# Kernel tuning notes

Measured on AMD Instinct MI355X. Metric: run time of the kernel, lower is better.

## Reference

```python
import jax, jax.numpy as jnp
import numpy as np

N_NODES = 50000
N_EDGES = 800000
FEAT = 128
HID = 128
NUM_GRAPHS = 64
ODE_STEPS = 8   # fixed-step RK4 stand-in for adaptive odeint over CFG.ode_time_points
DEPTH = 1.0
EPS = 1e-5


def layer_norm(x, g, b):
    m = jnp.mean(x, axis=-1, keepdims=True)
    v = jnp.var(x, axis=-1, keepdims=True)
    return (x - m) * jax.lax.rsqrt(v + EPS) * g + b


def setup_inputs() -> dict:
    key = jax.random.key(0)
    ks = jax.random.split(key, 16)
    s = 1.0 / np.sqrt(FEAT)
    sh = 1.0 / np.sqrt(HID)
    inp = {
        "x": jax.random.normal(ks[0], (N_NODES, FEAT), jnp.float32),
        "edge_index": jax.random.randint(ks[1], (2, N_EDGES), 0, N_NODES, jnp.int64),
        "batch": jnp.sort(jax.random.randint(ks[2], (N_NODES,), 0, NUM_GRAPHS, jnp.int64)),
        "alpha": jnp.float32(0.8),
        "beta": jnp.float32(0.6),
        "phase": jnp.float32(0.7),
        "W_in": jax.random.normal(ks[3], (FEAT, HID), jnp.float32) * s,
        "b_in": jnp.zeros((HID,), jnp.float32),
        "g_in": jnp.ones((HID,), jnp.float32),
        "be_in": jnp.zeros((HID,), jnp.float32),
        "W_alt": jax.random.normal(ks[4], (FEAT, HID), jnp.float32) * s,
        "b_alt": jnp.zeros((HID,), jnp.float32),
        "g_alt": jnp.ones((HID,), jnp.float32),
        "be_alt": jnp.zeros((HID,), jnp.float32),
        "W_self": jax.random.normal(ks[5], (HID, HID), jnp.float32) * sh,
        "W_msg": jax.random.normal(ks[6], (HID, HID), jnp.float32) * sh,
        "b_ode": jnp.zeros((HID,), jnp.float32),
        "W_int": jax.random.normal(ks[7], (2 * HID, HID), jnp.float32) * sh / np.sqrt(2.0),
        "b_int": jnp.zeros((HID,), jnp.float32),
        "g_int": jnp.ones((HID,), jnp.float32),
        "be_int": jnp.zeros((HID,), jnp.float32),
        "W_out": jax.random.normal(ks[8], (HID, HID), jnp.float32) * sh,
        "b_out": jnp.zeros((HID,), jnp.float32),
    }
    return inp


def _forward(x, alpha, beta, phase,
             W_in, b_in, g_in, be_in,
             W_alt, b_alt, g_alt, be_alt,
             W_self, W_msg, b_ode,
             W_int, b_int, g_int, be_int,
             W_out, b_out,
             edge_index, batch):
    src, dst = edge_index[0], edge_index[1]
    # in-degree for mean aggregation (clamped to 1)
    deg = jax.ops.segment_sum(jnp.ones((src.shape[0],), jnp.float32), dst,
                              num_segments=N_NODES)
    deg = jnp.maximum(deg, 1.0)[:, None]

    # quantum amplitudes -> measurement probabilities (normalized)
    norm = jnp.sqrt(alpha ** 2 + beta ** 2)
    a, b = alpha / norm, beta / norm
    p0, p1 = a ** 2, b ** 2

    # two projection pathways in superposition
    h0 = jax.nn.gelu(layer_norm(x @ W_in + b_in, g_in, be_in))
    h1 = jax.nn.gelu(layer_norm(x @ W_alt + b_alt, g_alt, be_alt))
    h = jnp.sqrt(p0) * h0 + jnp.sqrt(p1) * h1  # [N, H]

    # Neural ODE: dh/dt = tanh(h W_self + mean_{j->i}(h_j W_msg) + b)
    def ode_f(h):
        msg = h[src] @ W_msg                       # [E, H] gather + GEMM
        agg = jax.ops.segment_sum(msg, dst, num_segments=N_NODES) / deg
        return jnp.tanh(h @ W_self + agg + b_ode)

    dt = jnp.float32(DEPTH / ODE_STEPS)

    def rk4_step(h, _):
        k1 = ode_f(h)
        k2 = ode_f(h + 0.5 * dt * k1)
        k3 = ode_f(h + 0.5 * dt * k2)
        k4 = ode_f(h + dt * k3)
        return h + (dt / 6.0) * (k1 + 2.0 * k2 + 2.0 * k3 + k4), None

    h, _ = jax.lax.scan(rk4_step, h, None, length=ODE_STEPS)

    # quantum interference mixing (conditional branch -> masked add)
    interf = 2.0 * jnp.sqrt(p0 * p1) * jnp.cos(phase)
    h_int = jnp.tanh(layer_norm(jnp.concatenate([h, h], axis=-1) @ W_int + b_int,
                                g_int, be_int))
    gate = jnp.where(jnp.abs(interf) > 0.01, interf, 0.0)
    h = h + gate * h_int

    # eval-mode collapse: if p1 >= p0, scale by Re(e^{i*phase}) = cos(phase)
    h = jnp.where(p0 > p1, h, h * jnp.cos(phase))

    h_out = h @ W_out + b_out

    # global mean pool over graphs
    cnt = jax.ops.segment_sum(jnp.ones((N_NODES,), jnp.float32), batch,
                              num_segments=NUM_GRAPHS)
    pooled = jax.ops.segment_sum(h_out, batch, num_segments=NUM_GRAPHS)
    return pooled / jnp.maximum(cnt, 1.0)[:, None]  # [NUM_GRAPHS, H]


def reference(x, edge_index, batch, alpha, beta, phase,
              W_in, b_in, g_in, be_in,
              W_alt, b_alt, g_alt, be_alt,
              W_self, W_msg, b_ode,
              W_int, b_int, g_int, be_int,
              W_out, b_out):
    return _forward(x, alpha, beta, phase,
                    W_in, b_in, g_in, be_in,
                    W_alt, b_alt, g_alt, be_alt,
                    W_self, W_msg, b_ode,
                    W_int, b_int, g_int, be_int,
                    W_out, b_out, edge_index, batch)
```

## Files before the change

### kernel.cpp

```cpp
#include <hip/hip_runtime.h>
#include <math.h>

#define NND 50000
#define NED 800000
#define HD  128
#define NG  64
#define MT  32

typedef __attribute__((ext_vector_type(8))) short short8v;
typedef __attribute__((ext_vector_type(4))) float float4v;
typedef __attribute__((ext_vector_type(2))) float float2v;

__device__ __forceinline__ float gelu_t(float x) {
  const float c = 0.7978845608028654f;
  float t = tanhf(c * (x + 0.044715f * x * x * x));
  return 0.5f * x * (1.0f + t);
}

__device__ __forceinline__ unsigned short f2bf(float f) {
  unsigned int u = __float_as_uint(f);
  u += 0x7FFFu + ((u >> 16) & 1u);
  return (unsigned short)(u >> 16);
}
__device__ __forceinline__ float bf2f(unsigned short s) {
  return __uint_as_float(((unsigned int)s) << 16);
}
__device__ __forceinline__ float bflo(unsigned int u) { return __uint_as_float(u << 16); }
__device__ __forceinline__ float bfhi(unsigned int u) { return __uint_as_float(u & 0xFFFF0000u); }
__device__ __forceinline__ unsigned char f2fp8(float f) {
  return (unsigned char)(__builtin_amdgcn_cvt_pk_fp8_f32(f, f, 0, false) & 0xFF);
}

__global__ void k_hist(const int* __restrict__ dst, int* __restrict__ degi) {
  int e = blockIdx.x * 256 + threadIdx.x;
  if (e < NED) atomicAdd(&degi[dst[e]], 1);
}

__global__ __launch_bounds__(1024) void k_scan(
    const int* __restrict__ degi, int* __restrict__ rowptr,
    int* __restrict__ cursor, float* __restrict__ deginv) {
  __shared__ int wsum[16];
  int tid = threadIdx.x;
  int lane = tid & 63;
  int wid = tid >> 6;
  int running = 0;
  for (int base = 0; base < NND; base += 1024) {
    int idx = base + tid;
    int v = (idx < NND) ? degi[idx] : 0;
    int s = v;
#pragma unroll
    for (int o = 1; o < 64; o <<= 1) {
      int t = __shfl_up(s, o, 64);
      if (lane >= o) s += t;
    }
    if (lane == 63) wsum[wid] = s;
    __syncthreads();
    if (wid == 0) {
      int ws = (lane < 16) ? wsum[lane] : 0;
#pragma unroll
      for (int o = 1; o < 16; o <<= 1) {
        int t = __shfl_up(ws, o, 64);
        if (lane >= o) ws += t;
      }
      if (lane < 16) wsum[lane] = ws;
    }
    __syncthreads();
    int woff = wid ? wsum[wid - 1] : 0;
    int excl = running + woff + s - v;
    if (idx < NND) {
      rowptr[idx] = excl;
      cursor[idx] = excl;
      deginv[idx] = 1.0f / (float)max(v, 1);
    }
    int tot = wsum[15];
    __syncthreads();
    running += tot;
  }
  if (tid == 0) rowptr[NND] = running;
}

__global__ void k_scatter(const int* __restrict__ src, const int* __restrict__ dst,
                          int* __restrict__ cursor, int* __restrict__ csrsrc) {
  int e = blockIdx.x * 256 + threadIdx.x;
  if (e < NED) {
    int d = dst[e];
    int pos = atomicAdd(&cursor[d], 1);
    csrsrc[pos] = src[e];
  }
}

__global__ void k_cnt(const int* __restrict__ batch, float* __restrict__ cnt) {
  int g = threadIdx.x;
  if (g >= NG) return;
  int lo, hi, ub_g, ub_gm1;
  lo = 0; hi = NND;
  while (lo < hi) { int mid = (lo + hi) >> 1; if (batch[mid] <= g) lo = mid + 1; else hi = mid; }
  ub_g = lo;
  if (g == 0) ub_gm1 = 0;
  else {
    lo = 0; hi = NND;
    int v = g - 1;
    while (lo < hi) { int mid = (lo + hi) >> 1; if (batch[mid] <= v) lo = mid + 1; else hi = mid; }
    ub_gm1 = lo;
  }
  cnt[g] = (float)(ub_g - ub_gm1);
}

__global__ void k_weff(const float* __restrict__ Wint, float* __restrict__ weff) {
  int i = blockIdx.x * 256 + threadIdx.x;
  if (i < HD * HD) weff[i] = Wint[i] + Wint[i + HD * HD];
}

__global__ void k_prepB(const float* __restrict__ Wself, const float* __restrict__ Wmsg,
                        unsigned short* __restrict__ Bt) {
  int i = blockIdx.x * 256 + threadIdx.x;
  if (i < 128 * 256) {
    int n = i >> 8, k = i & 255;
    float w = (k < HD) ? Wself[k * HD + n] : Wmsg[(k - HD) * HD + n];
    Bt[i] = f2bf(w);
  }
}

__global__ void k_prepIn(const float* __restrict__ Win, const float* __restrict__ Walt,
                         unsigned short* __restrict__ BtIn) {
  int i = blockIdx.x * 256 + threadIdx.x;
  if (i < 2 * 128 * 128) {
    int p = i >> 14; int rem = i & 16383; int n = rem >> 7; int k = rem & 127;
    const float* W = p ? Walt : Win;
    BtIn[i] = f2bf(W[k * 128 + n]);
  }
}

__global__ __launch_bounds__(256) void k_init2(
    const float* __restrict__ x, const unsigned short* __restrict__ BtIn,
    const float* __restrict__ bin, const float* __restrict__ gin, const float* __restrict__ bein,
    const float* __restrict__ balt, const float* __restrict__ galt, const float* __restrict__ bealt,
    const float* __restrict__ alphap, const float* __restrict__ betap,
    float* __restrict__ hdst, unsigned short* __restrict__ hbf)
{
  __shared__ float red[4][16][2];
  __shared__ unsigned short gtile[2][16][64];
  int tid = threadIdx.x;
  int wave = tid >> 6;
  int lane = tid & 63;
  int l15 = lane & 15;
  int lhi = lane >> 4;
  int path = wave >> 1;
  int colBase = (wave & 1) * 64;
  int rowBase = blockIdx.x * 64;

  const unsigned short* Bp = BtIn + path * 128 * 128;
  short8v bfr[4][4];
#pragma unroll
  for (int t = 0; t < 4; ++t) {
    int n = colBase + t * 16 + l15;
#pragma unroll
    for (int s = 0; s < 4; ++s)
      bfr[t][s] = *(const short8v*)&Bp[n * 128 + s * 32 + lhi * 8];
  }

  const float* bvp = path ? balt : bin;
  const float* gp  = path ? galt : gin;
  const float* bep = path ? bealt : bein;
  float bv[4], gw[4], bew[4];
#pragma unroll
  for (int t = 0; t < 4; ++t) {
    int col = colBase + t * 16 + l15;
    bv[t] = bvp[col]; gw[t] = gp[col]; bew[t] = bep[col];
  }

  float al = alphap[0], btv = betap[0];
  float nrm = sqrtf(al * al + btv * btv);
  float w0 = fabsf(al) / nrm, w1 = fabsf(btv) / nrm;

  for (int rt = 0; rt < 4; ++rt) {
    int arow = rowBase + rt * 16 + l15; if (arow >= NND) arow = NND - 1;
    short8v afr[4];
#pragma unroll
    for (int s = 0; s < 4; ++s) {
      float4 xa = *(const float4*)&x[(size_t)arow * HD + s * 32 + lhi * 8];
      float4 xb = *(const float4*)&x[(size_t)arow * HD + s * 32 + lhi * 8 + 4];
      short8v f;
      f[0] = (short)f2bf(xa.x); f[1] = (short)f2bf(xa.y);
      f[2] = (short)f2bf(xa.z); f[3] = (short)f2bf(xa.w);
      f[4] = (short)f2bf(xb.x); f[5] = (short)f2bf(xb.y);
      f[6] = (short)f2bf(xb.z); f[7] = (short)f2bf(xb.w);
      afr[s] = f;
    }

    float4v acc[4];
#pragma unroll
    for (int t = 0; t < 4; ++t) acc[t] = (float4v){0.f, 0.f, 0.f, 0.f};
#pragma unroll
    for (int s = 0; s < 4; ++s) {
#pragma unroll
      for (int t = 0; t < 4; ++t)
        acc[t] = __builtin_amdgcn_mfma_f32_16x16x32_bf16(afr[s], bfr[t][s], acc[t], 0, 0, 0);
    }

    float z[4][4];
    float psum[4], psq[4];
#pragma unroll
    for (int r = 0; r < 4; ++r) {
      float s1 = 0.f, s2 = 0.f;
#pragma unroll
      for (int t = 0; t < 4; ++t) {
        float zz = acc[t][r] + bv[t];
        z[r][t] = zz;
        s1 += zz; s2 += zz * zz;
      }
#pragma unroll
      for (int m = 1; m < 16; m <<= 1) {
        s1 += __shfl_xor(s1, m, 16);
        s2 += __shfl_xor(s2, m, 16);
      }
      psum[r] = s1; psq[r] = s2;
    }
    if (l15 == 0) {
#pragma unroll
      for (int r = 0; r < 4; ++r) {
        red[wave][lhi * 4 + r][0] = psum[r];
        red[wave][lhi * 4 + r][1] = psq[r];
      }
    }
    __syncthreads();

    int pw = wave ^ 1;
    float gval[4][4];
#pragma unroll
    for (int r = 0; r < 4; ++r) {
      int rowl = lhi * 4 + r;
      float S = psum[r] + red[pw][rowl][0];
      float Q = psq[r]  + red[pw][rowl][1];
      float mean = S * (1.0f / 128.0f);
      float var  = Q * (1.0f / 128.0f) - mean * mean;
      float rs = rsqrtf(var + 1e-5f);
#pragma unroll
      for (int t = 0; t < 4; ++t)
        gval[r][t] = gelu_t((z[r][t] - mean) * rs * gw[t] + bew[t]);
    }

    if (path == 1) {
#pragma unroll
      for (int r = 0; r < 4; ++r)
#pragma unroll
        for (int t = 0; t < 4; ++t)
          gtile[wave & 1][lhi * 4 + r][t * 16 + l15] = f2bf(gval[r][t]);
    }
    __syncthreads();

    if (path == 0) {
#pragma unroll
      for (int r = 0; r < 4; ++r) {
        int m = rowBase + rt * 16 + lhi * 4 + r;
        if (m < NND) {
#pragma unroll
          for (int t = 0; t < 4; ++t) {
            float g1 = bf2f(gtile[wave & 1][lhi * 4 + r][t * 16 + l15]);
            float hv = w0 * gval[r][t] + w1 * g1;
            size_t off = (size_t)m * HD + colBase + t * 16 + l15;
            hdst[off] = hv;
            hbf[off] = f2bf(hv);
          }
        }
      }
    }
    __syncthreads();
  }
}

__global__ __launch_bounds__(256) void k_fused(
    const unsigned short* __restrict__ ain,
    const unsigned short* __restrict__ hbf,
    const unsigned char* __restrict__ k8r,
    unsigned char* __restrict__ k8w,
    unsigned short* __restrict__ usav,
    unsigned short* __restrict__ kacc,
    const int* __restrict__ rowptr, const int* __restrict__ csrsrc,
    const float* __restrict__ deginv,
    const unsigned short* __restrict__ Bt, const float* __restrict__ bode,
    float* __restrict__ hfp,
    unsigned short* __restrict__ ybf,
    unsigned short* __restrict__ hbfout, int stage)
{
  __shared__ unsigned char u_lds[MT * 256];
  int tid = threadIdx.x;
  int wave = tid >> 6;
  int lane = tid & 63;
  int l15 = lane & 15;
  int lhi = lane >> 4;
  int rowBase = blockIdx.x * MT;
  int ncol0 = wave * 32;

  const float DT = 0.125f;
  float wk = (stage == 0 || stage == 3) ? DT / 6.0f : DT / 3.0f;
  float cy = (stage <= 1) ? 0.5f * DT : DT;
  float cu = (stage == 3) ? DT : 0.5f * DT;

  if (stage == 0) {
    int l16 = tid & 15;
    int grp = tid >> 4;
#pragma unroll
    for (int g = 0; g < MT / 16; ++g) {
      int nloc = g * 16 + grp;
      int node = rowBase + nloc;
      if (node < NND) {
        int e0 = rowptr[node], e1 = rowptr[node + 1];
        float a0=0,a1=0,a2=0,a3=0,a4=0,a5=0,a6=0,a7=0;
        for (int eb = e0; eb < e1; eb += 8) {
          int n8 = e1 - eb; if (n8 > 8) n8 = 8;
          int sidx[8];
#pragma unroll
          for (int j = 0; j < 8; ++j) sidx[j] = csrsrc[eb + ((j < n8) ? j : 0)];
#pragma unroll
          for (int j = 0; j < 8; ++j) {
            if (j < n8) {
              uint4 v = *(const uint4*)&hbf[(size_t)sidx[j] * HD + l16 * 8];
              a0 += bflo(v.x); a1 += bfhi(v.x); a2 += bflo(v.y); a3 += bfhi(v.y);
              a4 += bflo(v.z); a5 += bfhi(v.z); a6 += bflo(v.w); a7 += bfhi(v.w);
            }
          }
        }
        float di = deginv[node];
        uint4 o;
        o.x = (unsigned int)f2bf(a0*di) | ((unsigned int)f2bf(a1*di) << 16);
        o.y = (unsigned int)f2bf(a2*di) | ((unsigned int)f2bf(a3*di) << 16);
        o.z = (unsigned int)f2bf(a4*di) | ((unsigned int)f2bf(a5*di) << 16);
        o.w = (unsigned int)f2bf(a6*di) | ((unsigned int)f2bf(a7*di) << 16);
        unsigned int boff = (unsigned int)nloc * 256u +
            (((unsigned int)l16 * 16u) ^ (((unsigned int)nloc & 7u) << 4));
        *(uint4*)&u_lds[boff] = o;
        *(uint4*)&usav[(size_t)node * HD + l16 * 8] = o;
      }
    }
  } else {
    int l8 = tid & 7;
    int grp = tid >> 3;
#pragma unroll
    for (int g = 0; g < MT / 32; ++g) {
      int nloc = g * 32 + grp;
      int node = rowBase + nloc;
      if (node < NND) {
        int e0 = rowptr[node], e1 = rowptr[node + 1];
        float a[16];
#pragma unroll
        for (int q = 0; q < 16; ++q) a[q] = 0.f;
        for (int eb = e0; eb < e1; eb += 8) {
          int n8 = e1 - eb; if (n8 > 8) n8 = 8;
          int sidx[8];
#pragma unroll
          for (int j = 0; j < 8; ++j) sidx[j] = csrsrc[eb + ((j < n8) ? j : 0)];
#pragma unroll
          for (int j = 0; j < 8; ++j) {
            if (j < n8) {
              uint4 v = *(const uint4*)&k8r[(size_t)sidx[j] * HD + l8 * 16];
              float2v f0 = __builtin_amdgcn_cvt_pk_f32_fp8(v.x, false);
              float2v f1 = __builtin_amdgcn_cvt_pk_f32_fp8(v.x, true);
              float2v f2 = __builtin_amdgcn_cvt_pk_f32_fp8(v.y, false);
              float2v f3 = __builtin_amdgcn_cvt_pk_f32_fp8(v.y, true);
              float2v f4 = __builtin_amdgcn_cvt_pk_f32_fp8(v.z, false);
              float2v f5 = __builtin_amdgcn_cvt_pk_f32_fp8(v.z, true);
              float2v f6 = __builtin_amdgcn_cvt_pk_f32_fp8(v.w, false);
              float2v f7 = __builtin_amdgcn_cvt_pk_f32_fp8(v.w, true);
              a[0]+=f0[0]; a[1]+=f0[1]; a[2]+=f1[0]; a[3]+=f1[1];
              a[4]+=f2[0]; a[5]+=f2[1]; a[6]+=f3[0]; a[7]+=f3[1];
              a[8]+=f4[0]; a[9]+=f4[1]; a[10]+=f5[0]; a[11]+=f5[1];
              a[12]+=f6[0]; a[13]+=f6[1]; a[14]+=f7[0]; a[15]+=f7[1];
            }
          }
        }
        float di = deginv[node] * cu;
        uint4 us0 = *(const uint4*)&usav[(size_t)node * HD + l8 * 16];
        uint4 us1 = *(const uint4*)&usav[(size_t)node * HD + l8 * 16 + 8];
        float u0  = bflo(us0.x) + a[0]*di,  u1  = bfhi(us0.x) + a[1]*di;
        float u2  = bflo(us0.y) + a[2]*di,  u3  = bfhi(us0.y) + a[3]*di;
        float u4  = bflo(us0.z) + a[4]*di,  u5  = bfhi(us0.z) + a[5]*di;
        float u6  = bflo(us0.w) + a[6]*di,  u7  = bfhi(us0.w) + a[7]*di;
        float u8  = bflo(us1.x) + a[8]*di,  u9  = bfhi(us1.x) + a[9]*di;
        float u10 = bflo(us1.y) + a[10]*di, u11 = bfhi(us1.y) + a[11]*di;
        float u12 = bflo(us1.z) + a[12]*di, u13 = bfhi(us1.z) + a[13]*di;
        float u14 = bflo(us1.w) + a[14]*di, u15 = bfhi(us1.w) + a[15]*di;
        uint4 o0, o1;
        o0.x = (unsigned int)f2bf(u0)  | ((unsigned int)f2bf(u1)  << 16);
        o0.y = (unsigned int)f2bf(u2)  | ((unsigned int)f2bf(u3)  << 16);
        o0.z = (unsigned int)f2bf(u4)  | ((unsigned int)f2bf(u5)  << 16);
        o0.w = (unsigned int)f2bf(u6)  | ((unsigned int)f2bf(u7)  << 16);
        o1.x = (unsigned int)f2bf(u8)  | ((unsigned int)f2bf(u9)  << 16);
        o1.y = (unsigned int)f2bf(u10) | ((unsigned int)f2bf(u11) << 16);
        o1.z = (unsigned int)f2bf(u12) | ((unsigned int)f2bf(u13) << 16);
        o1.w = (unsigned int)f2bf(u14) | ((unsigned int)f2bf(u15) << 16);
        unsigned int base = (unsigned int)nloc * 256u;
        unsigned int sw = ((unsigned int)nloc & 7u) << 4;
        *(uint4*)&u_lds[base + (((unsigned int)l8 * 32u) ^ sw)] = o0;
        *(uint4*)&u_lds[base + (((unsigned int)l8 * 32u + 16u) ^ sw)] = o1;
      }
    }
  }

  short8v bfr[2][8];
#pragma unroll
  for (int t = 0; t < 2; ++t) {
    int n = ncol0 + t * 16 + l15;
#pragma unroll
    for (int s = 0; s < 8; ++s) {
      bfr[t][s] = *(const short8v*)&Bt[n * 256 + s * 32 + lhi * 8];
    }
  }
  float bo0 = bode[ncol0 + l15];
  float bo1 = bode[ncol0 + 16 + l15];

  __syncthreads();

#pragma unroll
  for (int rt = 0; rt < MT / 16; ++rt) {
    int rloc = rt * 16 + l15;
    int mload = rowBase + rloc;
    if (mload >= NND) mload = NND - 1;
    short8v afr[8];
#pragma unroll
    for (int s = 0; s < 4; ++s)
      afr[s] = *(const short8v*)&ain[(size_t)mload * HD + s * 32 + lhi * 8];
#pragma unroll
    for (int s = 0; s < 4; ++s) {
      unsigned int boff = (unsigned int)rloc * 256u +
        ((((unsigned int)s * 64u) + ((unsigned int)lhi * 16u)) ^ (((unsigned int)rloc & 7u) << 4));
      afr[4 + s] = *(const short8v*)&u_lds[boff];
    }

    float4v acc0 = {0.f, 0.f, 0.f, 0.f};
    float4v acc1 = {0.f, 0.f, 0.f, 0.f};
#pragma unroll
    for (int s = 0; s < 8; ++s) {
      acc0 = __builtin_amdgcn_mfma_f32_16x16x32_bf16(afr[s], bfr[0][s], acc0, 0, 0, 0);
      acc1 = __builtin_amdgcn_mfma_f32_16x16x32_bf16(afr[s], bfr[1][s], acc1, 0, 0, 0);
    }

#pragma unroll
    for (int t = 0; t < 2; ++t) {
      int n = ncol0 + t * 16 + l15;
      float bo = t ? bo1 : bo0;
#pragma unroll
      for (int r = 0; r < 4; ++r) {
        int m = rowBase + rt * 16 + lhi * 4 + r;
        if (m < NND) {
          size_t off = (size_t)m * HD + n;
          float av = t ? acc1[r] : acc0[r];
          float kv = tanhf(av + bo);
          if (stage == 0) {
            ybf[off] = f2bf(bf2f(hbf[off]) + cy * kv);
            kacc[off] = f2bf(wk * kv);
            k8w[off] = f2fp8(kv);
          } else if (stage < 3) {
            ybf[off] = f2bf(bf2f(hbf[off]) + cy * kv);
            kacc[off] = f2bf(bf2f(kacc[off]) + wk * kv);
            k8w[off] = f2fp8(kv);
          } else {
            float hn = hfp[off] + bf2f(kacc[off]) + wk * kv;
            hfp[off] = hn;
            hbfout[off] = f2bf(hn);
          }
        }
      }
    }
  }
}

__global__ __launch_bounds__(256) void k_interf(
    const float* __restrict__ h, const float* __restrict__ weff,
    const float* __restrict__ bint, const float* __restrict__ gint,
    const float* __restrict__ beint,
    const float* __restrict__ alphap, const float* __restrict__ betap,
    const float* __restrict__ phasep,
    float* __restrict__ h2out)
{
  __shared__ float As[64][16];
  __shared__ float Bs[16][128];
  int tid = threadIdx.x;
  int tx = tid & 31, ty = tid >> 5;
  int rowBase = blockIdx.x * 64;
  float acc[8][4];
#pragma unroll
  for (int i = 0; i < 8; ++i) { acc[i][0]=0.f; acc[i][1]=0.f; acc[i][2]=0.f; acc[i][3]=0.f; }

  for (int kc = 0; kc < 8; ++kc) {
    int k0 = kc * 16;
    {
      int r = tid >> 2, kq = (tid & 3) * 4;
      int row = rowBase + r; if (row >= NND) row = NND - 1;
      *(float4*)&As[r][kq] = *(const float4*)&h[(size_t)row * HD + k0 + kq];
    }
#pragma unroll
    for (int j = 0; j < 2; ++j) {
      int kk = (tid >> 5) + j * 8;
      int n = (tid & 31) * 4;
      *(float4*)&Bs[kk][n] = *(const float4*)&weff[(k0 + kk) * HD + n];
    }
    __syncthreads();
#pragma unroll
    for (int kq = 0; kq < 4; ++kq) {
      float4 b0 = *(float4*)&Bs[kq*4+0][tx*4];
      float4 b1 = *(float4*)&Bs[kq*4+1][tx*4];
      float4 b2 = *(float4*)&Bs[kq*4+2][tx*4];
      float4 b3 = *(float4*)&Bs[kq*4+3][tx*4];
#pragma unroll
      for (int i = 0; i < 8; ++i) {
        float4 a = *(float4*)&As[ty*8+i][kq*4];
        acc[i][0] = fmaf(a.x,b0.x,fmaf(a.y,b1.x,fmaf(a.z,b2.x,fmaf(a.w,b3.x,acc[i][0]))));
        acc[i][1] = fmaf(a.x,b0.y,fmaf(a.y,b1.y,fmaf(a.z,b2.y,fmaf(a.w,b3.y,acc[i][1]))));
        acc[i][2] = fmaf(a.x,b0.z,fmaf(a.y,b1.z,fmaf(a.z,b2.z,fmaf(a.w,b3.z,acc[i][2]))));
        acc[i][3] = fmaf(a.x,b0.w,fmaf(a.y,b1.w,fmaf(a.z,b2.w,fmaf(a.w,b3.w,acc[i][3]))));
      }
    }
    __syncthreads();
  }

  float al = alphap[0], bt = betap[0], ph = phasep[0];
  float n2 = al*al + bt*bt;
  float p0 = (al*al) / n2, p1 = (bt*bt) / n2;
  float interf = 2.0f * sqrtf(p0 * p1) * cosf(ph);
  float gate = (fabsf(interf) > 0.01f) ? interf : 0.0f;
  float cscale = (p0 > p1) ? 1.0f : cosf(ph);

  int c0 = tx * 4;
  float4 bi  = *(const float4*)&bint[c0];
  float4 gv  = *(const float4*)&gint[c0];
  float4 bev = *(const float4*)&beint[c0];
#pragma unroll
  for (int i = 0; i < 8; ++i) {
    int row = rowBase + ty*8 + i;
    float z0 = acc[i][0]+bi.x, z1 = acc[i][1]+bi.y, z2 = acc[i][2]+bi.z, z3 = acc[i][3]+bi.w;
    float rsum = z0+z1+z2+z3;
    float rsq  = z0*z0+z1*z1+z2*z2+z3*z3;
#pragma unroll
    for (int m = 1; m < 32; m <<= 1) { rsum += __shfl_xor(rsum, m, 32); rsq += __shfl_xor(rsq, m, 32); }
    float mean = rsum * (1.0f/128.0f);
    float var  = rsq * (1.0f/128.0f) - mean*mean;
    float rs = rsqrtf(var + 1e-5f);
    float t0 = tanhf((z0-mean)*rs*gv.x + bev.x);
    float t1 = tanhf((z1-mean)*rs*gv.y + bev.y);
    float t2 = tanhf((z2-mean)*rs*gv.z + bev.z);
    float t3 = tanhf((z3-mean)*rs*gv.w + bev.w);
    if (row < NND) {
      size_t off = (size_t)row * HD + c0;
      float4 hv = *(const float4*)&h[off];
      float4 o = make_float4((hv.x + gate*t0) * cscale,
                             (hv.y + gate*t1) * cscale,
                             (hv.z + gate*t2) * cscale,
                             (hv.w + gate*t3) * cscale);
      *(float4*)&h2out[off] = o;
    }
  }
}

__global__ __launch_bounds__(256) void k_out(
    const float* __restrict__ h2, const float* __restrict__ Wout,
    const float* __restrict__ bout, const int* __restrict__ batch,
    float* __restrict__ pooled)
{
  __shared__ float As[64][16];
  __shared__ float Bs[16][128];
  int tid = threadIdx.x;
  int tx = tid & 31, ty = tid >> 5;
  int rowBase = blockIdx.x * 64;
  float acc[8][4];
#pragma unroll
  for (int i = 0; i < 8; ++i) { acc[i][0]=0.f; acc[i][1]=0.f; acc[i][2]=0.f; acc[i][3]=0.f; }

  for (int kc = 0; kc < 8; ++kc) {
    int k0 = kc * 16;
    {
      int r = tid >> 2, kq = (tid & 3) * 4;
      int row = rowBase + r; if (row >= NND) row = NND - 1;
      *(float4*)&As[r][kq] = *(const float4*)&h2[(size_t)row * HD + k0 + kq];
    }
#pragma unroll
    for (int j = 0; j < 2; ++j) {
      int kk = (tid >> 5) + j * 8;
      int n = (tid & 31) * 4;
      *(float4*)&Bs[kk][n] = *(const float4*)&Wout[(k0 + kk) * HD + n];
    }
    __syncthreads();
#pragma unroll
    for (int kq = 0; kq < 4; ++kq) {
      float4 b0 = *(float4*)&Bs[kq*4+0][tx*4];
      float4 b1 = *(float4*)&Bs[kq*4+1][tx*4];
      float4 b2 = *(float4*)&Bs[kq*4+2][tx*4];
      float4 b3 = *(float4*)&Bs[kq*4+3][tx*4];
#pragma unroll
      for (int i = 0; i < 8; ++i) {
        float4 a = *(float4*)&As[ty*8+i][kq*4];
        acc[i][0] = fmaf(a.x,b0.x,fmaf(a.y,b1.x,fmaf(a.z,b2.x,fmaf(a.w,b3.x,acc[i][0]))));
        acc[i][1] = fmaf(a.x,b0.y,fmaf(a.y,b1.y,fmaf(a.z,b2.y,fmaf(a.w,b3.y,acc[i][1]))));
        acc[i][2] = fmaf(a.x,b0.z,fmaf(a.y,b1.z,fmaf(a.z,b2.z,fmaf(a.w,b3.z,acc[i][2]))));
        acc[i][3] = fmaf(a.x,b0.w,fmaf(a.y,b1.w,fmaf(a.z,b2.w,fmaf(a.w,b3.w,acc[i][3]))));
      }
    }
    __syncthreads();
  }

  int c0 = tx * 4;
  float4 bo = *(const float4*)&bout[c0];
  int prevg = -1;
  float r0 = 0.f, r1 = 0.f, r2 = 0.f, r3 = 0.f;
#pragma unroll
  for (int i = 0; i < 8; ++i) {
    int row = rowBase + ty*8 + i;
    if (row >= NND) break;
    int g = batch[row];
    float v0 = acc[i][0] + bo.x;
    float v1 = acc[i][1] + bo.y;
    float v2 = acc[i][2] + bo.z;
    float v3 = acc[i][3] + bo.w;
    if (g != prevg) {
      if (prevg >= 0) {
        atomicAdd(&pooled[prevg*HD + c0 + 0], r0);
        atomicAdd(&pooled[prevg*HD + c0 + 1], r1);
        atomicAdd(&pooled[prevg*HD + c0 + 2], r2);
        atomicAdd(&pooled[prevg*HD + c0 + 3], r3);
      }
      prevg = g; r0 = v0; r1 = v1; r2 = v2; r3 = v3;
    } else {
      r0 += v0; r1 += v1; r2 += v2; r3 += v3;
    }
  }
  if (prevg >= 0) {
    atomicAdd(&pooled[prevg*HD + c0 + 0], r0);
    atomicAdd(&pooled[prevg*HD + c0 + 1], r1);
    atomicAdd(&pooled[prevg*HD + c0 + 2], r2);
    atomicAdd(&pooled[prevg*HD + c0 + 3], r3);
  }
}

__global__ void k_final(const float* __restrict__ pooled, const float* __restrict__ cnt,
                        float* __restrict__ out) {
  int i = blockIdx.x * 256 + threadIdx.x;
  if (i < NG * HD) out[i] = pooled[i] / fmaxf(cnt[i >> 7], 1.0f);
}

extern "C" void kernel_launch(void* const* d_in, const int* in_sizes, int n_in,
                              void* d_out, int out_size, void* d_ws, size_t ws_size,
                              hipStream_t stream) {
  (void)in_sizes; (void)n_in; (void)out_size; (void)ws_size;
  const float* x     = (const float*)d_in[0];
  const int*   ei    = (const int*)d_in[1];
  const int*   batch = (const int*)d_in[2];
  const float* alpha = (const float*)d_in[3];
  const float* beta  = (const float*)d_in[4];
  const float* phase = (const float*)d_in[5];
  const float* Win   = (const float*)d_in[6];
  const float* bin   = (const float*)d_in[7];
  const float* gin   = (const float*)d_in[8];
  const float* bein  = (const float*)d_in[9];
  const float* Walt  = (const float*)d_in[10];
  const float* balt  = (const float*)d_in[11];
  const float* galt  = (const float*)d_in[12];
  const float* bealt = (const float*)d_in[13];
  const float* Wself = (const float*)d_in[14];
  const float* Wmsg  = (const float*)d_in[15];
  const float* bode  = (const float*)d_in[16];
  const float* Wint  = (const float*)d_in[17];
  const float* bint  = (const float*)d_in[18];
  const float* gint  = (const float*)d_in[19];
  const float* beint = (const float*)d_in[20];
  const float* Wout  = (const float*)d_in[21];
  const float* bout  = (const float*)d_in[22];
  float* out = (float*)d_out;

  const int* esrc = ei;
  const int* edst = ei + NED;

  size_t NH = (size_t)NND * HD;
  float* h      = (float*)d_ws;
  float* h2     = h + NH;
  float* deginv = h2 + NH;
  float* weff   = deginv + NND;
  float* pooled = weff + HD * HD;
  float* cnt    = pooled + NG * HD;
  unsigned short* hbf  = (unsigned short*)(cnt + NG);
  unsigned short* ybf  = hbf + NH;
  unsigned short* usav = ybf + NH;
  unsigned short* kacc = usav + NH;
  unsigned short* Bt   = kacc + NH;
  unsigned short* BtIn = Bt + 128 * 256;
  unsigned char* k8a = (unsigned char*)(BtIn + 2 * 128 * 128);
  unsigned char* k8b = k8a + NH;
  int* degi   = (int*)(k8b + NH);
  int* rowptr = degi + NND;
  int* cursor = rowptr + (NND + 4);
  int* csrsrc = cursor + NND;

  hipMemsetAsync(degi, 0, NND * sizeof(int), stream);
  hipMemsetAsync(pooled, 0, NG * HD * sizeof(float), stream);

  k_hist   <<<(NED + 255) / 256, 256, 0, stream>>>(edst, degi);
  k_scan   <<<1, 1024, 0, stream>>>(degi, rowptr, cursor, deginv);
  k_scatter<<<(NED + 255) / 256, 256, 0, stream>>>(esrc, edst, cursor, csrsrc);
  k_cnt    <<<1, 64, 0, stream>>>(batch, cnt);
  k_weff   <<<(HD * HD + 255) / 256, 256, 0, stream>>>(Wint, weff);
  k_prepB  <<<128, 256, 0, stream>>>(Wself, Wmsg, Bt);
  k_prepIn <<<128, 256, 0, stream>>>(Win, Walt, BtIn);
  k_init2  <<<(NND + 63) / 64, 256, 0, stream>>>(x, BtIn, bin, gin, bein,
                                                 balt, galt, bealt,
                                                 alpha, beta, h, hbf);
  int nblk = (NND + MT - 1) / MT;
  for (int step = 0; step < 8; ++step) {
    for (int stage = 0; stage < 4; ++stage) {
      const unsigned short* ain = (stage == 0) ? hbf : ybf;
      const unsigned char* k8r = (stage == 2) ? k8b : k8a;
      unsigned char* k8w = (stage == 1) ? k8b : k8a;
      k_fused<<<nblk, 256, 0, stream>>>(ain, hbf, k8r, k8w, usav, kacc,
                                        rowptr, csrsrc, deginv, Bt, bode,
                                        h, ybf, hbf, stage);
    }
  }
  k_interf<<<(NND + 63) / 64, 256, 0, stream>>>(h, weff, bint, gint, beint,
                                                alpha, beta, phase, h2);
  k_out   <<<(NND + 63) / 64, 256, 0, stream>>>(h2, Wout, bout, batch, pooled);
  k_final <<<(NG * HD + 255) / 256, 256, 0, stream>>>(pooled, cnt, out);
}
```

Before: 2.332 ms.

## Keep ODE state in bf16, reuse aggregated dh for next step's stage-0 gather

The fp32 master copy of h is dropped and the state lives only in bf16. Each step's final stage now writes the fp8-scaled increment dh, so the next step's first stage updates the saved aggregate u by adding the mean of dh over neighbours, using linearity. The full bf16 gather over h is no longer recomputed. Neighbour index loads are made cooperative through lane shuffles with 16-edge batches and all loads issued before converting, and the row tile grows to 64. This trades accumulation precision (bf16 state, fp8 increments, drift in u across steps) for less gather and store traffic.

```diff
diff --git a/kernel.cpp b/kernel.cpp
--- a/kernel.cpp
+++ b/kernel.cpp
@@ -5,7 +5,7 @@
 #define NED 800000
 #define HD  128
 #define NG  64
-#define MT  32
+#define MT  64
 
 typedef __attribute__((ext_vector_type(8))) short short8v;
 typedef __attribute__((ext_vector_type(4))) float float4v;
@@ -136,7 +136,7 @@
     const float* __restrict__ bin, const float* __restrict__ gin, const float* __restrict__ bein,
     const float* __restrict__ balt, const float* __restrict__ galt, const float* __restrict__ bealt,
     const float* __restrict__ alphap, const float* __restrict__ betap,
-    float* __restrict__ hdst, unsigned short* __restrict__ hbf)
+    unsigned short* __restrict__ hbf)
 {
   __shared__ float red[4][16][2];
   __shared__ unsigned short gtile[2][16][64];
@@ -258,9 +258,7 @@
           for (int t = 0; t < 4; ++t) {
             float g1 = bf2f(gtile[wave & 1][lhi * 4 + r][t * 16 + l15]);
             float hv = w0 * gval[r][t] + w1 * g1;
-            size_t off = (size_t)m * HD + colBase + t * 16 + l15;
-            hdst[off] = hv;
-            hbf[off] = f2bf(hv);
+            hbf[(size_t)m * HD + colBase + t * 16 + l15] = f2bf(hv);
           }
         }
       }
@@ -271,17 +269,16 @@
 
 __global__ __launch_bounds__(256) void k_fused(
     const unsigned short* __restrict__ ain,
-    const unsigned short* __restrict__ hbf,
-    const unsigned char* __restrict__ k8r,
+    unsigned short* __restrict__ hbf,
+    const unsigned char* __restrict__ gsrc8,
     unsigned char* __restrict__ k8w,
+    unsigned char* __restrict__ dh8,
     unsigned short* __restrict__ usav,
     unsigned short* __restrict__ kacc,
     const int* __restrict__ rowptr, const int* __restrict__ csrsrc,
     const float* __restrict__ deginv,
     const unsigned short* __restrict__ Bt, const float* __restrict__ bode,
-    float* __restrict__ hfp,
-    unsigned short* __restrict__ ybf,
-    unsigned short* __restrict__ hbfout, int stage)
+    unsigned short* __restrict__ ybf, int mode)
 {
   __shared__ unsigned char u_lds[MT * 256];
   int tid = threadIdx.x;
@@ -293,11 +290,8 @@
   int ncol0 = wave * 32;
 
   const float DT = 0.125f;
-  float wk = (stage == 0 || stage == 3) ? DT / 6.0f : DT / 3.0f;
-  float cy = (stage <= 1) ? 0.5f * DT : DT;
-  float cu = (stage == 3) ? DT : 0.5f * DT;
-
-  if (stage == 0) {
+
+  if (mode == 0) {
     int l16 = tid & 15;
     int grp = tid >> 4;
 #pragma unroll
@@ -307,15 +301,16 @@
       if (node < NND) {
         int e0 = rowptr[node], e1 = rowptr[node + 1];
         float a0=0,a1=0,a2=0,a3=0,a4=0,a5=0,a6=0,a7=0;
-        for (int eb = e0; eb < e1; eb += 8) {
-          int n8 = e1 - eb; if (n8 > 8) n8 = 8;
-          int sidx[8];
-#pragma unroll
-          for (int j = 0; j < 8; ++j) sidx[j] = csrsrc[eb + ((j < n8) ? j : 0)];
-#pragma unroll
-          for (int j = 0; j < 8; ++j) {
-            if (j < n8) {
-              uint4 v = *(const uint4*)&hbf[(size_t)sidx[j] * HD + l16 * 8];
+        for (int eb = e0; eb < e1; eb += 16) {
+          int rem = e1 - eb;
+          int idx0 = eb + ((l16 < rem) ? l16 : rem - 1);
+          int my = csrsrc[idx0];
+          int n16 = (rem < 16) ? rem : 16;
+#pragma unroll
+          for (int j = 0; j < 16; ++j) {
+            if (j < n16) {
+              int s = __shfl(my, j, 16);
+              uint4 v = *(const uint4*)&hbf[(size_t)s * HD + l16 * 8];
               a0 += bflo(v.x); a1 += bfhi(v.x); a2 += bflo(v.y); a3 += bfhi(v.y);
               a4 += bflo(v.z); a5 += bfhi(v.z); a6 += bflo(v.w); a7 += bfhi(v.w);
             }
@@ -334,6 +329,7 @@
       }
     }
   } else {
+    float dscale = (mode == 1) ? 0.125f : ((mode == 4) ? DT : 0.5f * DT);
     int l8 = tid & 7;
     int grp = tid >> 3;
 #pragma unroll
@@ -345,23 +341,30 @@
         float a[16];
 #pragma unroll
         for (int q = 0; q < 16; ++q) a[q] = 0.f;
-        for (int eb = e0; eb < e1; eb += 8) {
-          int n8 = e1 - eb; if (n8 > 8) n8 = 8;
-          int sidx[8];
-#pragma unroll
-          for (int j = 0; j < 8; ++j) sidx[j] = csrsrc[eb + ((j < n8) ? j : 0)];
-#pragma unroll
-          for (int j = 0; j < 8; ++j) {
-            if (j < n8) {
-              uint4 v = *(const uint4*)&k8r[(size_t)sidx[j] * HD + l8 * 16];
-              float2v f0 = __builtin_amdgcn_cvt_pk_f32_fp8(v.x, false);
-              float2v f1 = __builtin_amdgcn_cvt_pk_f32_fp8(v.x, true);
-              float2v f2 = __builtin_amdgcn_cvt_pk_f32_fp8(v.y, false);
-              float2v f3 = __builtin_amdgcn_cvt_pk_f32_fp8(v.y, true);
-              float2v f4 = __builtin_amdgcn_cvt_pk_f32_fp8(v.z, false);
-              float2v f5 = __builtin_amdgcn_cvt_pk_f32_fp8(v.z, true);
-              float2v f6 = __builtin_amdgcn_cvt_pk_f32_fp8(v.w, false);
-              float2v f7 = __builtin_amdgcn_cvt_pk_f32_fp8(v.w, true);
+        for (int eb = e0; eb < e1; eb += 16) {
+          int rem = e1 - eb;
+          int my0 = csrsrc[eb + ((l8 < rem) ? l8 : rem - 1)];
+          int my1 = (rem > 8) ? csrsrc[eb + 8 + ((l8 < rem - 8) ? l8 : rem - 9)] : 0;
+          int n16 = (rem < 16) ? rem : 16;
+          uint4 v[16];
+#pragma unroll
+          for (int j = 0; j < 16; ++j) {
+            if (j < n16) {
+              int s = (j < 8) ? __shfl(my0, j, 8) : __shfl(my1, j - 8, 8);
+              v[j] = *(const uint4*)&gsrc8[(size_t)s * HD + l8 * 16];
+            }
+          }
+#pragma unroll
+          for (int j = 0; j < 16; ++j) {
+            if (j < n16) {
+              float2v f0 = __builtin_amdgcn_cvt_pk_f32_fp8(v[j].x, false);
+              float2v f1 = __builtin_amdgcn_cvt_pk_f32_fp8(v[j].x, true);
+              float2v f2 = __builtin_amdgcn_cvt_pk_f32_fp8(v[j].y, false);
+              float2v f3 = __builtin_amdgcn_cvt_pk_f32_fp8(v[j].y, true);
+              float2v f4 = __builtin_amdgcn_cvt_pk_f32_fp8(v[j].z, false);
+              float2v f5 = __builtin_amdgcn_cvt_pk_f32_fp8(v[j].z, true);
+              float2v f6 = __builtin_amdgcn_cvt_pk_f32_fp8(v[j].w, false);
+              float2v f7 = __builtin_amdgcn_cvt_pk_f32_fp8(v[j].w, true);
               a[0]+=f0[0]; a[1]+=f0[1]; a[2]+=f1[0]; a[3]+=f1[1];
               a[4]+=f2[0]; a[5]+=f2[1]; a[6]+=f3[0]; a[7]+=f3[1];
               a[8]+=f4[0]; a[9]+=f4[1]; a[10]+=f5[0]; a[11]+=f5[1];
@@ -369,7 +372,7 @@
             }
           }
         }
-        float di = deginv[node] * cu;
+        float di = deginv[node] * dscale;
         uint4 us0 = *(const uint4*)&usav[(size_t)node * HD + l8 * 16];
         uint4 us1 = *(const uint4*)&usav[(size_t)node * HD + l8 * 16 + 8];
         float u0  = bflo(us0.x) + a[0]*di,  u1  = bfhi(us0.x) + a[1]*di;
@@ -393,6 +396,10 @@
         unsigned int sw = ((unsigned int)nloc & 7u) << 4;
         *(uint4*)&u_lds[base + (((unsigned int)l8 * 32u) ^ sw)] = o0;
         *(uint4*)&u_lds[base + (((unsigned int)l8 * 32u + 16u) ^ sw)] = o1;
+        if (mode == 1) {
+          *(uint4*)&usav[(size_t)node * HD + l8 * 16] = o0;
+          *(uint4*)&usav[(size_t)node * HD + l8 * 16 + 8] = o1;
+        }
       }
     }
   }
@@ -410,6 +417,9 @@
   float bo1 = bode[ncol0 + 16 + l15];
 
   __syncthreads();
+
+  const float wk = (mode <= 1 || mode == 4) ? DT / 6.0f : DT / 3.0f;
+  const float cy = (mode <= 2) ? 0.5f * DT : DT;
 
 #pragma unroll
   for (int rt = 0; rt < MT / 16; ++rt) {
@@ -446,18 +456,19 @@
           size_t off = (size_t)m * HD + n;
           float av = t ? acc1[r] : acc0[r];
           float kv = tanhf(av + bo);
-          if (stage == 0) {
+          if (mode <= 1) {
             ybf[off] = f2bf(bf2f(hbf[off]) + cy * kv);
             kacc[off] = f2bf(wk * kv);
             k8w[off] = f2fp8(kv);
-          } else if (stage < 3) {
+          } else if (mode <= 3) {
             ybf[off] = f2bf(bf2f(hbf[off]) + cy * kv);
             kacc[off] = f2bf(bf2f(kacc[off]) + wk * kv);
             k8w[off] = f2fp8(kv);
           } else {
-            float hn = hfp[off] + bf2f(kacc[off]) + wk * kv;
-            hfp[off] = hn;
-            hbfout[off] = f2bf(hn);
+            float dh = bf2f(kacc[off]) + wk * kv;
+            float hn = bf2f(hbf[off]) + dh;
+            hbf[off] = f2bf(hn);
+            dh8[off] = f2fp8(8.0f * dh);
           }
         }
       }
@@ -466,7 +477,7 @@
 }
 
 __global__ __launch_bounds__(256) void k_interf(
-    const float* __restrict__ h, const float* __restrict__ weff,
+    const unsigned short* __restrict__ hbf, const float* __restrict__ weff,
     const float* __restrict__ bint, const float* __restrict__ gint,
     const float* __restrict__ beint,
     const float* __restrict__ alphap, const float* __restrict__ betap,
@@ -487,7 +498,9 @@
     {
       int r = tid >> 2, kq = (tid & 3) * 4;
       int row = rowBase + r; if (row >= NND) row = NND - 1;
-      *(float4*)&As[r][kq] = *(const float4*)&h[(size_t)row * HD + k0 + kq];
+      uint2 v = *(const uint2*)&hbf[(size_t)row * HD + k0 + kq];
+      As[r][kq+0] = bflo(v.x); As[r][kq+1] = bfhi(v.x);
+      As[r][kq+2] = bflo(v.y); As[r][kq+3] = bfhi(v.y);
     }
 #pragma unroll
     for (int j = 0; j < 2; ++j) {
@@ -542,11 +555,12 @@
     float t3 = tanhf((z3-mean)*rs*gv.w + bev.w);
     if (row < NND) {
       size_t off = (size_t)row * HD + c0;
-      float4 hv = *(const float4*)&h[off];
-      float4 o = make_float4((hv.x + gate*t0) * cscale,
-                             (hv.y + gate*t1) * cscale,
-                             (hv.z + gate*t2) * cscale,
-                             (hv.w + gate*t3) * cscale);
+      uint2 hv = *(const uint2*)&hbf[off];
+      float h0 = bflo(hv.x), h1 = bfhi(hv.x), h2 = bflo(hv.y), h3 = bfhi(hv.y);
+      float4 o = make_float4((h0 + gate*t0) * cscale,
+                             (h1 + gate*t1) * cscale,
+                             (h2 + gate*t2) * cscale,
+                             (h3 + gate*t3) * cscale);
       *(float4*)&h2out[off] = o;
     }
   }
@@ -670,8 +684,7 @@
   const int* edst = ei + NED;
 
   size_t NH = (size_t)NND * HD;
-  float* h      = (float*)d_ws;
-  float* h2     = h + NH;
+  float* h2     = (float*)d_ws;
   float* deginv = h2 + NH;
   float* weff   = deginv + NND;
   float* pooled = weff + HD * HD;
@@ -684,7 +697,8 @@
   unsigned short* BtIn = Bt + 128 * 256;
   unsigned char* k8a = (unsigned char*)(BtIn + 2 * 128 * 128);
   unsigned char* k8b = k8a + NH;
-  int* degi   = (int*)(k8b + NH);
+  unsigned char* dh8 = k8b + NH;
+  int* degi   = (int*)(dh8 + NH);
   int* rowptr = degi + NND;
   int* cursor = rowptr + (NND + 4);
   int* csrsrc = cursor + NND;
@@ -701,19 +715,23 @@
   k_prepIn <<<128, 256, 0, stream>>>(Win, Walt, BtIn);
   k_init2  <<<(NND + 63) / 64, 256, 0, stream>>>(x, BtIn, bin, gin, bein,
                                                  balt, galt, bealt,
-                                                 alpha, beta, h, hbf);
+                                                 alpha, beta, hbf);
   int nblk = (NND + MT - 1) / MT;
   for (int step = 0; step < 8; ++step) {
-    for (int stage = 0; stage < 4; ++stage) {
-      const unsigned short* ain = (stage == 0) ? hbf : ybf;
-      const unsigned char* k8r = (stage == 2) ? k8b : k8a;
-      unsigned char* k8w = (stage == 1) ? k8b : k8a;
-      k_fused<<<nblk, 256, 0, stream>>>(ain, hbf, k8r, k8w, usav, kacc,
-                                        rowptr, csrsrc, deginv, Bt, bode,
-                                        h, ybf, hbf, stage);
-    }
-  }
-  k_interf<<<(NND + 63) / 64, 256, 0, stream>>>(h, weff, bint, gint, beint,
+    k_fused<<<nblk, 256, 0, stream>>>(hbf, hbf, dh8, k8a, dh8, usav, kacc,
+                                      rowptr, csrsrc, deginv, Bt, bode,
+                                      ybf, (step == 0) ? 0 : 1);
+    k_fused<<<nblk, 256, 0, stream>>>(ybf, hbf, k8a, k8b, dh8, usav, kacc,
+                                      rowptr, csrsrc, deginv, Bt, bode,
+                                      ybf, 2);
+    k_fused<<<nblk, 256, 0, stream>>>(ybf, hbf, k8b, k8a, dh8, usav, kacc,
+                                      rowptr, csrsrc, deginv, Bt, bode,
+                                      ybf, 3);
+    k_fused<<<nblk, 256, 0, stream>>>(ybf, hbf, k8a, k8b, dh8, usav, kacc,
+                                      rowptr, csrsrc, deginv, Bt, bode,
+                                      ybf, 4);
+  }
+  k_interf<<<(NND + 63) / 64, 256, 0, stream>>>(hbf, weff, bint, gint, beint,
                                                 alpha, beta, phase, h2);
   k_out   <<<(NND + 63) / 64, 256, 0, stream>>>(h2, Wout, bout, batch, pooled);
   k_final <<<(NG * HD + 255) / 256, 256, 0, stream>>>(pooled, cnt, out);
```

Result: faster. 2.029 ms (-13.0%).
